# Performance work log

Measured on AMD Instinct MI355X. Metric: run time of the kernel, lower is better.

The kernel has to match this reference:

```python
import jax, jax.numpy as jnp
import numpy as np

N = 24000      # total nodes (8000 per node type)
IN_DIM = 128
OUT_DIM = 128
H = 8          # heads
DK = 16        # out_dim // n_heads
T = 3          # node types (hard-coded in edge_attention)
R = 34         # relations (etypes 0..33 per the etype->ntype rules)
EPR = 10000    # edges per relation (DGL applies edge fn per etype)


def _rel_node_types(num_rel):
    # src/dst node type per relation, transcribed from edge_attention
    src_nt = np.array([0 if r <= 9 else (1 if r <= 21 else 2) for r in range(num_rel)], np.int32)
    def _dnt(r):
        if r <= 2 or 10 <= r <= 13 or 22 <= r <= 24:
            return 0
        if 3 <= r <= 6 or 14 <= r <= 17 or 25 <= r <= 28:
            return 1
        return 2
    dst_nt = np.array([_dnt(r) for r in range(num_rel)], np.int32)
    return src_nt, dst_nt

SRC_NT, DST_NT = _rel_node_types(R)


def setup_inputs() -> dict:
    rng = np.random.default_rng(0)
    Nt = N // T  # nodes of type t live in [t*Nt, (t+1)*Nt)
    src = np.stack([rng.integers(SRC_NT[r] * Nt, (SRC_NT[r] + 1) * Nt, EPR) for r in range(R)]).astype(np.int32)
    dst = np.stack([rng.integers(DST_NT[r] * Nt, (DST_NT[r] + 1) * Nt, EPR) for r in range(R)]).astype(np.int32)
    ks = jax.random.split(jax.random.key(0), 10)
    lin = 1.0 / np.sqrt(IN_DIM)
    return {
        'x': jax.random.normal(ks[0], (N, IN_DIM), jnp.float32),
        'src': jnp.asarray(src),
        'dst': jnp.asarray(dst),
        'Wk': jax.random.normal(ks[1], (T, IN_DIM, OUT_DIM), jnp.float32) * lin,
        'bk': jnp.zeros((T, OUT_DIM), jnp.float32),
        'Wq': jax.random.normal(ks[2], (T, IN_DIM, OUT_DIM), jnp.float32) * lin,
        'bq': jnp.zeros((T, OUT_DIM), jnp.float32),
        'Wv': jax.random.normal(ks[3], (T, IN_DIM, OUT_DIM), jnp.float32) * lin,
        'bv': jnp.zeros((T, OUT_DIM), jnp.float32),
        'Wa': jax.random.normal(ks[4], (T, OUT_DIM, OUT_DIM), jnp.float32) * lin,
        'ba': jnp.zeros((T, OUT_DIM), jnp.float32),
        'rel_att': jax.random.normal(ks[5], (R, H, DK, DK), jnp.float32) / np.sqrt(DK),
        'rel_msg': jax.random.normal(ks[6], (R, H, DK, DK), jnp.float32) / np.sqrt(DK),
        'rel_pri': jnp.ones((R, H), jnp.float32),
        'nta': jnp.ones((T,), jnp.float32),
        'nta1': jnp.ones((T,), jnp.float32),
        'skip': jnp.ones((T,), jnp.float32),
        'weight': jnp.ones((1,), jnp.float32),
        'attn_w': jax.random.normal(ks[7], (2 * DK,), jnp.float32) * 0.1,
    }


def reference(x, src, dst, Wk, bk, Wq, bq, Wv, bv, Wa, ba, rel_att, rel_msg, rel_pri, nta, nta1, skip, weight, attn_w):
    ntype = jnp.repeat(jnp.arange(T), N // T)  # node type per node id
    ridx = jnp.arange(N)

    def typed_lin(h, W, b):
        # per-node-type Linear: compute all T projections, select by node type
        return (jnp.einsum('ni,tio->tno', h, W) + b[:, None, :])[ntype, ridx]

    k = typed_lin(x, Wk, bk).reshape(N, H, DK)
    q = typed_lin(x, Wq, bq).reshape(N, H, DK)
    v = typed_lin(x, Wv, bv).reshape(N, H, DK)

    k_src = k[src]                                   # [R, Epr, H, DK]
    q_dst = q[dst]                                   # [R, Epr, H, DK]
    key_t = jnp.einsum('rehd,rhdf->rehf', k_src, rel_att)
    a = (q_dst * key_t).sum(-1) * rel_pri[:, None, :] / np.sqrt(DK)   # [R, Epr, H]
    val = jnp.einsum('rehd,rhdf->rehf', v[src], rel_msg)              # [R, Epr, H, DK]

    # GAT-style concat attention: attn_fc(cat(att_dst*q, att_src*k)) split into two dots
    wq, wk = attn_w[:DK], attn_w[DK:]
    na = jax.nn.leaky_relu(nta1[DST_NT][:, None, None] * (q_dst @ wq)
                           + nta[SRC_NT][:, None, None] * (k_src @ wk))  # [R, Epr, H]

    beta = jax.nn.sigmoid(weight[0])
    s = (a + beta * na).reshape(R * EPR, H)

    # per-(relation, dst-node) segment softmax (DGL mailbox softmax per etype)
    seg = (jnp.arange(R)[:, None] * N + dst).reshape(-1)
    m = jax.ops.segment_max(s, seg, num_segments=R * N)
    e = jnp.exp(s - m[seg])
    den = jax.ops.segment_sum(e, seg, num_segments=R * N)
    att = e / den[seg]

    vf = val.reshape(R * EPR, H, DK)
    h = jax.ops.segment_sum(att[:, :, None] * vf, seg, num_segments=R * N).reshape(R, N, OUT_DIM)

    # cross_reducer='mean': average over relations that delivered messages to a node
    cnt = jax.ops.segment_sum(jnp.ones((R * EPR,), x.dtype), seg, num_segments=R * N).reshape(R, N)
    nrel = jnp.maximum((cnt > 0).astype(x.dtype).sum(0), 1.0)
    t = h.sum(0) / nrel[:, None]                      # [N, OUT_DIM]

    trans = (jnp.einsum('no,top->tnp', t, Wa) + ba[:, None, :])[ntype, ridx]
    alpha = jax.nn.sigmoid(skip)[ntype][:, None]
    return trans * alpha + x * (1.0 - alpha)
```

## Files before the change

### kernel.cpp

```cpp
#include <hip/hip_runtime.h>

#define NN   24000
#define NTP  8000
#define HH   8
#define DKK  16
#define RR   34
#define EPRN 10000
#define NE   (RR*EPRN)
#define NB   (RR*NTP)
#define CAP  16

typedef short short8 __attribute__((ext_vector_type(8)));
typedef float f32x4  __attribute__((ext_vector_type(4)));

__device__ __forceinline__ int src_nt(int r){ return r<=9?0:(r<=21?1:2); }
__device__ __forceinline__ int dst_nt(int r){
    if (r<=2)  return 0;
    if (r<=6)  return 1;
    if (r<=9)  return 2;
    if (r<=13) return 0;
    if (r<=17) return 1;
    if (r<=21) return 2;
    if (r<=24) return 0;
    if (r<=28) return 1;
    return 2;
}

__device__ __forceinline__ unsigned short bf16rne(float a){
    unsigned int u = __float_as_uint(a);
    u += 0x7fffu + ((u >> 16) & 1u);
    return (unsigned short)(u >> 16);
}
__device__ __forceinline__ unsigned int bf2pack(float a, float b){
    unsigned int ua = __float_as_uint(a);
    unsigned int ub = __float_as_uint(b);
    ua += 0x7fffu + ((ua >> 16) & 1u);
    ub += 0x7fffu + ((ub >> 16) & 1u);
    return (ua >> 16) | (ub & 0xffff0000u);
}
__device__ __forceinline__ void unpack8(uint4 u, float* o){
    o[0] = __uint_as_float(u.x << 16); o[1] = __uint_as_float(u.x & 0xffff0000u);
    o[2] = __uint_as_float(u.y << 16); o[3] = __uint_as_float(u.y & 0xffff0000u);
    o[4] = __uint_as_float(u.z << 16); o[5] = __uint_as_float(u.z & 0xffff0000u);
    o[6] = __uint_as_float(u.w << 16); o[7] = __uint_as_float(u.w & 0xffff0000u);
}

__global__ __launch_bounds__(256) void prep_kernel(
    const float* __restrict__ Wk, const float* __restrict__ Wq,
    const float* __restrict__ Wv,
    int* __restrict__ counts, unsigned short* __restrict__ wfrag)
{
    const int gid = blockIdx.x * 256 + threadIdx.x;
    if (gid < NB) counts[gid] = 0;
    if (blockIdx.x < 72) {
        const int tile = blockIdx.x * 4 + (threadIdx.x >> 6);
        const int lane = threadIdx.x & 63;
        const int s   = tile & 3;
        const int n   = (tile >> 2) & 7;
        const int mat = (tile >> 5) % 3;
        const int tau = tile / 96;
        const float* W = (mat == 0 ? Wk : (mat == 1 ? Wq : Wv)) + (size_t)tau * 16384;
        const int k0  = s * 32 + (lane >> 4) * 8;
        const int col = n * 16 + (lane & 15);
        unsigned short* dstp = wfrag + (size_t)tile * 512 + lane * 8;
        #pragma unroll
        for (int i = 0; i < 8; i++)
            dstp[i] = bf16rne(W[(size_t)(k0 + i) * 128 + col]);
    }
}

__global__ __launch_bounds__(256) void qkv_mfma(
    const float* __restrict__ x,
    const float* __restrict__ bk, const float* __restrict__ bq,
    const float* __restrict__ bv,
    const unsigned short* __restrict__ wfrag,
    float* __restrict__ qo, unsigned short* __restrict__ kvb)
{
    const int rb   = blockIdx.x * 64;
    const int tau  = rb / NTP;
    const int w    = threadIdx.x >> 6;
    const int lane = threadIdx.x & 63;
    const int m    = lane & 15;
    const int quad = lane >> 4;

    short8 af[4];
    {
        const float* xrow = x + (size_t)(rb + w * 16 + m) * 128;
        #pragma unroll
        for (int s = 0; s < 4; s++) {
            float4 f0 = *(const float4*)(xrow + s * 32 + quad * 8);
            float4 f1 = *(const float4*)(xrow + s * 32 + quad * 8 + 4);
            union { unsigned int u[4]; short8 v; } pk;
            pk.u[0] = bf2pack(f0.x, f0.y); pk.u[1] = bf2pack(f0.z, f0.w);
            pk.u[2] = bf2pack(f1.x, f1.y); pk.u[3] = bf2pack(f1.z, f1.w);
            af[s] = pk.v;
        }
    }

    #pragma unroll
    for (int mat = 0; mat < 3; mat++) {
        const float* bias = (mat == 0 ? bk : (mat == 1 ? bq : bv)) + tau * 128;
        #pragma unroll
        for (int n = 0; n < 8; n++) {
            float bb = bias[n * 16 + m];
            f32x4 acc = {bb, bb, bb, bb};
            #pragma unroll
            for (int s = 0; s < 4; s++) {
                const int tile = ((tau * 3 + mat) * 8 + n) * 4 + s;
                short8 bf = *(const short8*)(wfrag + (size_t)tile * 512 + lane * 8);
                acc = __builtin_amdgcn_mfma_f32_16x16x32_bf16(af[s], bf, acc, 0, 0, 0);
            }
            if (mat == 1) {
                #pragma unroll
                for (int i = 0; i < 4; i++)
                    qo[(size_t)(rb + w * 16 + quad * 4 + i) * 128 + n * 16 + m] = acc[i];
            } else {
                const int off = n * 32 + (mat == 0 ? 0 : 16) + m;
                #pragma unroll
                for (int i = 0; i < 4; i++)
                    kvb[(size_t)(rb + w * 16 + quad * 4 + i) * 256 + off] = bf16rne(acc[i]);
            }
        }
    }
}

__global__ __launch_bounds__(256) void scatter_fixed(
    const int* __restrict__ src, const int* __restrict__ dst,
    int* __restrict__ counts, int* __restrict__ esrc16)
{
    int e = blockIdx.x * 256 + threadIdx.x;
    if (e >= NE) return;
    int r = e / EPRN;
    int b = r * NTP + (dst[e] - dst_nt(r) * NTP);
    int pos = atomicAdd(&counts[b], 1);
    if (pos < CAP) esrc16[(size_t)b * CAP + pos] = src[e];
}

__global__ __launch_bounds__(256) void edge_fused(
    const float* __restrict__ q, const unsigned short* __restrict__ kvb,
    const int* __restrict__ esrc16, const int* __restrict__ counts,
    const float* __restrict__ rel_att, const float* __restrict__ rel_msg,
    const float* __restrict__ rel_pri,
    const float* __restrict__ nta, const float* __restrict__ nta1,
    const float* __restrict__ weightp, const float* __restrict__ attn_w,
    float* __restrict__ t_acc)
{
    const int tid  = threadIdx.x;
    const int h    = __builtin_amdgcn_readfirstlane((tid >> 6) + 4 * blockIdx.y);
    const int dn   = blockIdx.x * 64 + (tid & 63);
    const int dtau = __builtin_amdgcn_readfirstlane(dn / NTP);
    const int dl   = dn - dtau * NTP;

    float q16[16];
    {
        const float4* qp = (const float4*)(q + (size_t)dn * 128 + h * 16);
        #pragma unroll
        for (int i = 0; i < 4; i++) ((float4*)q16)[i] = qp[i];
    }
    float qwq = 0.f;
    #pragma unroll
    for (int f = 0; f < 16; f++) qwq += q16[f] * attn_w[f];
    const float c1   = nta1[dtau];
    const float beta = 1.f / (1.f + expf(-weightp[0]));

    float th[16] = {};
    int nrel = 0;

    for (int r = 0; r < RR; r++) {
        if (dst_nt(r) != dtau) continue;
        const int b   = r * NTP + dl;
        const int beg = b * CAP;
        int cnt = counts[b];
        cnt = cnt < CAP ? cnt : CAP;
        if (!__any(cnt > 0)) continue;

        const float* Ah = rel_att + (((size_t)r * HH + h) << 8);
        float Aq[16];
        #pragma unroll
        for (int d = 0; d < 16; d++) {
            float s = 0.f;
            #pragma unroll
            for (int f = 0; f < 16; f++) s += Ah[d * 16 + f] * q16[f];
            Aq[d] = s;
        }

        const float pri = rel_pri[r * HH + h] * 0.25f;
        const float c0  = nta[src_nt(r)];

        int4 e0 = *(const int4*)(esrc16 + beg);
        int4 e1 = *(const int4*)(esrc16 + beg + 4);
        int4 e2 = make_int4(0,0,0,0), e3 = make_int4(0,0,0,0);
        if (__any(cnt > 8)) {
            e2 = *(const int4*)(esrc16 + beg + 8);
            e3 = *(const int4*)(esrc16 + beg + 12);
        }

        float den = 0.f;
        float macc[16] = {};
        #pragma unroll
        for (int ch = 0; ch < 4; ch++) {
            if (!__any(ch * 4 < cnt)) break;
            const int4 cc = (ch == 0) ? e0 : (ch == 1) ? e1 : (ch == 2) ? e2 : e3;
            #pragma unroll
            for (int t = 0; t < 4; t++) {
                const int j = ch * 4 + t;
                if (j < cnt) {
                    const int sn = (t == 0) ? cc.x : (t == 1) ? cc.y : (t == 2) ? cc.z : cc.w;
                    const uint4* kp = (const uint4*)(kvb + (size_t)sn * 256 + h * 32);
                    uint4 u0 = kp[0], u1 = kp[1], u2 = kp[2], u3 = kp[3];
                    float kk[16], vv[16];
                    unpack8(u0, kk); unpack8(u1, kk + 8);
                    unpack8(u2, vv); unpack8(u3, vv + 8);
                    float a = 0.f, kwk = 0.f;
                    #pragma unroll
                    for (int d = 0; d < 16; d++) { a += kk[d] * Aq[d]; kwk += kk[d] * attn_w[16 + d]; }
                    float nax = c1 * qwq + c0 * kwk;
                    float na  = nax >= 0.f ? nax : 0.01f * nax;
                    float es  = expf(a * pri + beta * na);
                    den += es;
                    #pragma unroll
                    for (int f = 0; f < 16; f++) macc[f] += es * vv[f];
                }
            }
        }

        if (cnt > 0) {
            nrel++;
            const float inv = 1.f / den;
            const float* Mh = rel_msg + (((size_t)r * HH + h) << 8);
            #pragma unroll
            for (int d = 0; d < 16; d++) {
                float md = macc[d] * inv;
                #pragma unroll
                for (int f = 0; f < 16; f++) th[f] += md * Mh[d * 16 + f];
            }
        }
    }

    const float innv = 1.f / (float)(nrel > 1 ? nrel : 1);
    float* op = t_acc + (size_t)dn * 128 + h * 16;
    #pragma unroll
    for (int i = 0; i < 4; i++) {
        float4 o;
        o.x = th[i*4+0] * innv; o.y = th[i*4+1] * innv;
        o.z = th[i*4+2] * innv; o.w = th[i*4+3] * innv;
        *(float4*)(op + i * 4) = o;
    }
}

__global__ __launch_bounds__(256) void final_gemm(
    const float* __restrict__ t_acc,
    const float* __restrict__ Wa, const float* __restrict__ ba,
    const float* __restrict__ skip, const float* __restrict__ x,
    float* __restrict__ out)
{
    __shared__ float xT[16][68];
    __shared__ float wS[16][128];
    const int rb  = blockIdx.x * 64;
    const int tau = rb / NTP;
    const int tid = threadIdx.x;
    const float* W = Wa + (size_t)tau * 128 * 128;
    const int cg = tid & 31;
    const int rg = tid >> 5;
    float acc[8][4] = {};
    for (int kb = 0; kb < 128; kb += 16) {
        {
            int row = tid >> 2, kq = (tid & 3) * 4;
            float4 xv = *(const float4*)(t_acc + (size_t)(rb + row) * 128 + kb + kq);
            xT[kq+0][row] = xv.x; xT[kq+1][row] = xv.y;
            xT[kq+2][row] = xv.z; xT[kq+3][row] = xv.w;
        }
        {
            #pragma unroll
            for (int i = 0; i < 2; i++) {
                int f = tid + i * 256; int kk = f >> 5; int c4 = (f & 31) * 4;
                *(float4*)(&wS[kk][c4]) = *(const float4*)(W + (size_t)(kb + kk) * 128 + c4);
            }
        }
        __syncthreads();
        #pragma unroll
        for (int kk = 0; kk < 16; kk++) {
            float4 wv = *(const float4*)(&wS[kk][cg * 4]);
            float xr[8];
            *(float4*)&xr[0] = *(const float4*)(&xT[kk][rg * 8]);
            *(float4*)&xr[4] = *(const float4*)(&xT[kk][rg * 8 + 4]);
            #pragma unroll
            for (int j = 0; j < 8; j++) {
                acc[j][0] += xr[j] * wv.x; acc[j][1] += xr[j] * wv.y;
                acc[j][2] += xr[j] * wv.z; acc[j][3] += xr[j] * wv.w;
            }
        }
        __syncthreads();
    }
    float alpha = 1.f / (1.f + expf(-skip[tau]));
    float oma = 1.f - alpha;
    #pragma unroll
    for (int j = 0; j < 8; j++) {
        int row = rb + rg * 8 + j;
        float4 xv = *(const float4*)(x + (size_t)row * 128 + cg * 4);
        float4 o;
        o.x = (acc[j][0] + ba[tau*128 + cg*4+0]) * alpha + xv.x * oma;
        o.y = (acc[j][1] + ba[tau*128 + cg*4+1]) * alpha + xv.y * oma;
        o.z = (acc[j][2] + ba[tau*128 + cg*4+2]) * alpha + xv.z * oma;
        o.w = (acc[j][3] + ba[tau*128 + cg*4+3]) * alpha + xv.w * oma;
        *(float4*)(out + (size_t)row * 128 + cg * 4) = o;
    }
}

extern "C" void kernel_launch(void* const* d_in, const int* in_sizes, int n_in,
                              void* d_out, int out_size, void* d_ws, size_t ws_size,
                              hipStream_t stream) {
    const float* x       = (const float*)d_in[0];
    const int*   src     = (const int*)  d_in[1];
    const int*   dst     = (const int*)  d_in[2];
    const float* Wk      = (const float*)d_in[3];
    const float* bk      = (const float*)d_in[4];
    const float* Wq      = (const float*)d_in[5];
    const float* bq      = (const float*)d_in[6];
    const float* Wv      = (const float*)d_in[7];
    const float* bv      = (const float*)d_in[8];
    const float* Wa      = (const float*)d_in[9];
    const float* ba      = (const float*)d_in[10];
    const float* rel_att = (const float*)d_in[11];
    const float* rel_msg = (const float*)d_in[12];
    const float* rel_pri = (const float*)d_in[13];
    const float* nta     = (const float*)d_in[14];
    const float* nta1    = (const float*)d_in[15];
    const float* skip    = (const float*)d_in[16];
    const float* weight  = (const float*)d_in[17];
    const float* attn_w  = (const float*)d_in[18];
    float* out = (float*)d_out;

    float* ws    = (float*)d_ws;
    float* q     = ws;
    unsigned short* kvb = (unsigned short*)(q + (size_t)NN * 128);
    float* t_acc = (float*)(kvb + (size_t)NN * 256);
    int* counts  = (int*)(t_acc + (size_t)NN * 128);
    int* esrc16  = counts + NB;
    unsigned short* wfrag = (unsigned short*)(esrc16 + (size_t)NB * CAP);

    prep_kernel<<<1088, 256, 0, stream>>>(Wk, Wq, Wv, counts, wfrag);
    qkv_mfma<<<NN / 64, 256, 0, stream>>>(x, bk, bq, bv, wfrag, q, kvb);
    scatter_fixed<<<(NE + 255) / 256, 256, 0, stream>>>(src, dst, counts, esrc16);
    edge_fused<<<dim3(NN / 64, 2), 256, 0, stream>>>(
        q, kvb, esrc16, counts, rel_att, rel_msg, rel_pri,
        nta, nta1, weight, attn_w, t_acc);
    final_gemm<<<NN / 64, 256, 0, stream>>>(t_acc, Wa, ba, skip, x, out);
}
```

Baseline: 237.8 us.

## Use bf16 MFMA for final projection and stage QKV stores through LDS

Replaces the fp32 LDS-tiled final GEMM with a bf16 MFMA kernel that reuses prepacked Wa fragments built in prep_kernel. The edge kernel now writes its aggregated output as bf16, halving that intermediate's traffic. The QKV kernel stages its Q and K/V tiles in shared memory so global stores become coalesced 16-byte vectors instead of scattered scalars. Precision drops to bf16 for the final projection input, and the extra LDS use and barriers in qkv_mfma may lower occupancy.

```diff
diff --git a/kernel.cpp b/kernel.cpp
--- a/kernel.cpp
+++ b/kernel.cpp
@@ -47,19 +47,29 @@
 
 __global__ __launch_bounds__(256) void prep_kernel(
     const float* __restrict__ Wk, const float* __restrict__ Wq,
-    const float* __restrict__ Wv,
+    const float* __restrict__ Wv, const float* __restrict__ Wa,
     int* __restrict__ counts, unsigned short* __restrict__ wfrag)
 {
     const int gid = blockIdx.x * 256 + threadIdx.x;
     if (gid < NB) counts[gid] = 0;
-    if (blockIdx.x < 72) {
+    if (blockIdx.x < 96) {
         const int tile = blockIdx.x * 4 + (threadIdx.x >> 6);
         const int lane = threadIdx.x & 63;
-        const int s   = tile & 3;
-        const int n   = (tile >> 2) & 7;
-        const int mat = (tile >> 5) % 3;
-        const int tau = tile / 96;
-        const float* W = (mat == 0 ? Wk : (mat == 1 ? Wq : Wv)) + (size_t)tau * 16384;
+        const float* W;
+        int s, n;
+        if (tile < 288) {
+            s = tile & 3;
+            n = (tile >> 2) & 7;
+            const int mat = (tile >> 5) % 3;
+            const int tau = tile / 96;
+            W = (mat == 0 ? Wk : (mat == 1 ? Wq : Wv)) + (size_t)tau * 16384;
+        } else {
+            const int t2 = tile - 288;
+            s = t2 & 3;
+            n = (t2 >> 2) & 7;
+            const int tau = t2 >> 5;
+            W = Wa + (size_t)tau * 16384;
+        }
         const int k0  = s * 32 + (lane >> 4) * 8;
         const int col = n * 16 + (lane & 15);
         unsigned short* dstp = wfrag + (size_t)tile * 512 + lane * 8;
@@ -76,6 +86,8 @@
     const unsigned short* __restrict__ wfrag,
     float* __restrict__ qo, unsigned short* __restrict__ kvb)
 {
+    __shared__ float qs[4][16][132];
+    __shared__ unsigned short ksh[4][16][264];
     const int rb   = blockIdx.x * 64;
     const int tau  = rb / NTP;
     const int w    = threadIdx.x >> 6;
@@ -112,15 +124,31 @@
             }
             if (mat == 1) {
                 #pragma unroll
-                for (int i = 0; i < 4; i++)
-                    qo[(size_t)(rb + w * 16 + quad * 4 + i) * 128 + n * 16 + m] = acc[i];
+                for (int i = 0; i < 4; i++) qs[w][quad * 4 + i][n * 16 + m] = acc[i];
             } else {
                 const int off = n * 32 + (mat == 0 ? 0 : 16) + m;
                 #pragma unroll
-                for (int i = 0; i < 4; i++)
-                    kvb[(size_t)(rb + w * 16 + quad * 4 + i) * 256 + off] = bf16rne(acc[i]);
-            }
-        }
+                for (int i = 0; i < 4; i++) ksh[w][quad * 4 + i][off] = bf16rne(acc[i]);
+            }
+        }
+        if (mat == 1) {
+            __syncthreads();
+            #pragma unroll
+            for (int j = 0; j < 8; j++) {
+                const int id = lane + 64 * j;
+                const int row = id >> 5, c4 = id & 31;
+                float4 v = *(const float4*)(&qs[w][row][c4 * 4]);
+                *(float4*)(qo + (size_t)(rb + w * 16 + row) * 128 + c4 * 4) = v;
+            }
+        }
+    }
+    __syncthreads();
+    #pragma unroll
+    for (int j = 0; j < 8; j++) {
+        const int id = lane + 64 * j;
+        const int row = id >> 5, c8 = id & 31;
+        uint4 u = *(const uint4*)(&ksh[w][row][c8 * 8]);
+        *(uint4*)(kvb + (size_t)(rb + w * 16 + row) * 256 + c8 * 8) = u;
     }
 }
 
@@ -143,7 +171,7 @@
     const float* __restrict__ rel_pri,
     const float* __restrict__ nta, const float* __restrict__ nta1,
     const float* __restrict__ weightp, const float* __restrict__ attn_w,
-    float* __restrict__ t_acc)
+    unsigned short* __restrict__ t_bf)
 {
     const int tid  = threadIdx.x;
     const int h    = __builtin_amdgcn_readfirstlane((tid >> 6) + 4 * blockIdx.y);
@@ -238,72 +266,58 @@
     }
 
     const float innv = 1.f / (float)(nrel > 1 ? nrel : 1);
-    float* op = t_acc + (size_t)dn * 128 + h * 16;
+    unsigned short* op = t_bf + (size_t)dn * 128 + h * 16;
+    uint4 u0, u1;
+    u0.x = bf2pack(th[0] * innv,  th[1] * innv);
+    u0.y = bf2pack(th[2] * innv,  th[3] * innv);
+    u0.z = bf2pack(th[4] * innv,  th[5] * innv);
+    u0.w = bf2pack(th[6] * innv,  th[7] * innv);
+    u1.x = bf2pack(th[8] * innv,  th[9] * innv);
+    u1.y = bf2pack(th[10] * innv, th[11] * innv);
+    u1.z = bf2pack(th[12] * innv, th[13] * innv);
+    u1.w = bf2pack(th[14] * innv, th[15] * innv);
+    *(uint4*)(op)     = u0;
+    *(uint4*)(op + 8) = u1;
+}
+
+__global__ __launch_bounds__(256) void final_mfma(
+    const unsigned short* __restrict__ t_bf,
+    const unsigned short* __restrict__ wfrag,
+    const float* __restrict__ ba, const float* __restrict__ skip,
+    const float* __restrict__ x, float* __restrict__ out)
+{
+    const int rb   = blockIdx.x * 64;
+    const int tau  = rb / NTP;
+    const int w    = threadIdx.x >> 6;
+    const int lane = threadIdx.x & 63;
+    const int m    = lane & 15;
+    const int quad = lane >> 4;
+
+    short8 af[4];
+    {
+        const unsigned short* trow = t_bf + (size_t)(rb + w * 16 + m) * 128;
+        #pragma unroll
+        for (int s = 0; s < 4; s++)
+            af[s] = *(const short8*)(trow + s * 32 + quad * 8);
+    }
+    const float alpha = 1.f / (1.f + expf(-skip[tau]));
+    const float oma   = 1.f - alpha;
+
     #pragma unroll
-    for (int i = 0; i < 4; i++) {
-        float4 o;
-        o.x = th[i*4+0] * innv; o.y = th[i*4+1] * innv;
-        o.z = th[i*4+2] * innv; o.w = th[i*4+3] * innv;
-        *(float4*)(op + i * 4) = o;
-    }
-}
-
-__global__ __launch_bounds__(256) void final_gemm(
-    const float* __restrict__ t_acc,
-    const float* __restrict__ Wa, const float* __restrict__ ba,
-    const float* __restrict__ skip, const float* __restrict__ x,
-    float* __restrict__ out)
-{
-    __shared__ float xT[16][68];
-    __shared__ float wS[16][128];
-    const int rb  = blockIdx.x * 64;
-    const int tau = rb / NTP;
-    const int tid = threadIdx.x;
-    const float* W = Wa + (size_t)tau * 128 * 128;
-    const int cg = tid & 31;
-    const int rg = tid >> 5;
-    float acc[8][4] = {};
-    for (int kb = 0; kb < 128; kb += 16) {
-        {
-            int row = tid >> 2, kq = (tid & 3) * 4;
-            float4 xv = *(const float4*)(t_acc + (size_t)(rb + row) * 128 + kb + kq);
-            xT[kq+0][row] = xv.x; xT[kq+1][row] = xv.y;
-            xT[kq+2][row] = xv.z; xT[kq+3][row] = xv.w;
-        }
-        {
-            #pragma unroll
-            for (int i = 0; i < 2; i++) {
-                int f = tid + i * 256; int kk = f >> 5; int c4 = (f & 31) * 4;
-                *(float4*)(&wS[kk][c4]) = *(const float4*)(W + (size_t)(kb + kk) * 128 + c4);
-            }
-        }
-        __syncthreads();
-        #pragma unroll
-        for (int kk = 0; kk < 16; kk++) {
-            float4 wv = *(const float4*)(&wS[kk][cg * 4]);
-            float xr[8];
-            *(float4*)&xr[0] = *(const float4*)(&xT[kk][rg * 8]);
-            *(float4*)&xr[4] = *(const float4*)(&xT[kk][rg * 8 + 4]);
-            #pragma unroll
-            for (int j = 0; j < 8; j++) {
-                acc[j][0] += xr[j] * wv.x; acc[j][1] += xr[j] * wv.y;
-                acc[j][2] += xr[j] * wv.z; acc[j][3] += xr[j] * wv.w;
-            }
-        }
-        __syncthreads();
-    }
-    float alpha = 1.f / (1.f + expf(-skip[tau]));
-    float oma = 1.f - alpha;
-    #pragma unroll
-    for (int j = 0; j < 8; j++) {
-        int row = rb + rg * 8 + j;
-        float4 xv = *(const float4*)(x + (size_t)row * 128 + cg * 4);
-        float4 o;
-        o.x = (acc[j][0] + ba[tau*128 + cg*4+0]) * alpha + xv.x * oma;
-        o.y = (acc[j][1] + ba[tau*128 + cg*4+1]) * alpha + xv.y * oma;
-        o.z = (acc[j][2] + ba[tau*128 + cg*4+2]) * alpha + xv.z * oma;
-        o.w = (acc[j][3] + ba[tau*128 + cg*4+3]) * alpha + xv.w * oma;
-        *(float4*)(out + (size_t)row * 128 + cg * 4) = o;
+    for (int n = 0; n < 8; n++) {
+        float bb = ba[tau * 128 + n * 16 + m];
+        f32x4 acc = {bb, bb, bb, bb};
+        #pragma unroll
+        for (int s = 0; s < 4; s++) {
+            const int tile = 288 + tau * 32 + n * 4 + s;
+            short8 bf = *(const short8*)(wfrag + (size_t)tile * 512 + lane * 8);
+            acc = __builtin_amdgcn_mfma_f32_16x16x32_bf16(af[s], bf, acc, 0, 0, 0);
+        }
+        #pragma unroll
+        for (int i = 0; i < 4; i++) {
+            const size_t idx = (size_t)(rb + w * 16 + quad * 4 + i) * 128 + n * 16 + m;
+            out[idx] = acc[i] * alpha + x[idx] * oma;
+        }
     }
 }
 
@@ -334,16 +348,16 @@
     float* ws    = (float*)d_ws;
     float* q     = ws;
     unsigned short* kvb = (unsigned short*)(q + (size_t)NN * 128);
-    float* t_acc = (float*)(kvb + (size_t)NN * 256);
-    int* counts  = (int*)(t_acc + (size_t)NN * 128);
+    unsigned short* t_bf = kvb + (size_t)NN * 256;
+    int* counts  = (int*)(t_bf + (size_t)NN * 128);
     int* esrc16  = counts + NB;
     unsigned short* wfrag = (unsigned short*)(esrc16 + (size_t)NB * CAP);
 
-    prep_kernel<<<1088, 256, 0, stream>>>(Wk, Wq, Wv, counts, wfrag);
+    prep_kernel<<<1063, 256, 0, stream>>>(Wk, Wq, Wv, Wa, counts, wfrag);
     qkv_mfma<<<NN / 64, 256, 0, stream>>>(x, bk, bq, bv, wfrag, q, kvb);
     scatter_fixed<<<(NE + 255) / 256, 256, 0, stream>>>(src, dst, counts, esrc16);
     edge_fused<<<dim3(NN / 64, 2), 256, 0, stream>>>(
         q, kvb, esrc16, counts, rel_att, rel_msg, rel_pri,
-        nta, nta1, weight, attn_w, t_acc);
-    final_gemm<<<NN / 64, 256, 0, stream>>>(t_acc, Wa, ba, skip, x, out);
-}
+        nta, nta1, weight, attn_w, t_bf);
+    final_mfma<<<NN / 64, 256, 0, stream>>>(t_bf, wfrag, ba, skip, x, out);
+}
```

Result: no change. 235.9 us (-0.8%).
